# Kernel tuning notes

Measured on AMD Instinct MI355X. Metric: run time of the kernel, lower is better.

The kernel has to match this reference:

```python
import jax, jax.numpy as jnp
import numpy as np

EPS = 1e-6
CHI2_THRESH = 9.0
DIST_SCALE = 3.0


def _normalize(x, axis=1, eps=EPS):
    n = jnp.linalg.norm(x, axis=axis, keepdims=True)
    return x / jnp.maximum(n, eps)


def _skew(k):
    # k: (B,3) -> (B,3,3)
    kx, ky, kz = k[:, 0], k[:, 1], k[:, 2]
    O = jnp.zeros_like(kx)
    row0 = jnp.stack([O, -kz, ky], axis=1)
    row1 = jnp.stack([kz, O, -kx], axis=1)
    row2 = jnp.stack([-ky, kx, O], axis=1)
    return jnp.stack([row0, row1, row2], axis=1)


def gravity_align(g_src, g_tgt, eps=EPS):
    # Rodrigues rotation aligning g_src to g_tgt, batch-safe.
    u = _normalize(g_src, eps=eps)
    v = _normalize(g_tgt, eps=eps)
    axis = jnp.cross(u, v)
    axis_norm = jnp.linalg.norm(axis, axis=1, keepdims=True)
    dot = jnp.clip(jnp.sum(u * v, axis=1, keepdims=True), -1.0, 1.0)
    parallel = axis_norm < 1e-6
    k = axis / (axis_norm + eps)
    theta = jnp.arccos(dot)
    sin_t, cos_t = jnp.sin(theta), jnp.cos(theta)
    K = _skew(k)
    I = jnp.eye(3, dtype=g_src.dtype)[None]
    R = I + sin_t[:, :, None] * K + (1.0 - cos_t)[:, :, None] * (K @ K)
    # anti-parallel branch (computed unconditionally, selected via where)
    ex = jnp.array([1.0, 0.0, 0.0], dtype=u.dtype)[None]
    ey = jnp.array([0.0, 1.0, 0.0], dtype=u.dtype)[None]
    use_ex = jnp.abs(u[:, 0:1]) < 0.9
    basis = jnp.where(use_ex, ex, ey)
    axis2 = _normalize(jnp.cross(u, basis), eps=eps)
    K2 = _skew(axis2)
    R_anti = I + 2.0 * (K2 @ K2)
    antipar = parallel & (dot < 0.0)
    R = jnp.where(antipar[:, :, None], R_anti, R)
    R = jnp.where((parallel & (dot > 0.0))[:, :, None], I, R)
    return R


def _lower_median(x, axis):
    # torch.median(dim): lower median for even length
    n = x.shape[axis]
    return jnp.sort(x, axis=axis).take(indices=(n - 1) // 2, axis=axis)


def setup_inputs() -> dict:
    key = jax.random.key(0)
    ks = jax.random.split(key, 8)
    B, N = 4, 4096
    src = jax.random.normal(ks[0], (B, 3, N), jnp.float32)
    tgt = jax.random.normal(ks[1], (B, 3, N), jnp.float32)
    src_n = _normalize(jax.random.normal(ks[2], (B, 3, N), jnp.float32))
    tgt_n = _normalize(jax.random.normal(ks[3], (B, 3, N), jnp.float32))
    g_p = jax.random.normal(ks[4], (B, 3), jnp.float32)
    g_q = jax.random.normal(ks[5], (B, 3), jnp.float32)
    k_p = jax.random.uniform(ks[6], (B, 1), jnp.float32) + 0.1
    k_q = jax.random.uniform(ks[7], (B, 1), jnp.float32) + 0.1
    return {"src": src, "tgt": tgt, "src_n": src_n, "tgt_n": tgt_n,
            "g_p": g_p, "k_p": k_p, "g_q": g_q, "k_q": k_q}


def reference(src, tgt, src_n, tgt_n, g_p, k_p, g_q, k_q):
    B, _, N = src.shape
    R_g = gravity_align(g_p, g_q)  # (B,3,3)
    src_rot = jnp.einsum('bij,bjn->bin', R_g, src)
    src_n_rot = jnp.einsum('bij,bjn->bin', R_g, src_n)
    t_center = tgt.mean(axis=2, keepdims=True) - src_rot.mean(axis=2, keepdims=True)
    src_init = src_rot + t_center  # (B,3,N)

    # squared pairwise distances: (B,N,N)
    inner = -2.0 * jnp.einsum('bcn,bcm->bnm', src_init, tgt)
    xx = jnp.sum(src_init ** 2, axis=1)[:, :, None]
    yy = jnp.sum(tgt ** 2, axis=1)[:, None, :]
    dist_pq = xx + inner + yy

    min_pq = jnp.min(dist_pq, axis=2)
    corr_p2q = jnp.argmin(dist_pq, axis=2)
    min_qp = jnp.min(dist_pq, axis=1)
    corr_q2p = jnp.argmin(dist_pq, axis=1)

    nn_d_p = jnp.sqrt(jnp.maximum(min_pq, 0.0) + EPS)
    nn_d_q = jnp.sqrt(jnp.maximum(min_qp, 0.0) + EPS)
    tau_p = DIST_SCALE * _lower_median(nn_d_p, axis=1)[:, None]
    tau_q = DIST_SCALE * _lower_median(nn_d_q, axis=1)[:, None]
    geom_p = (nn_d_p <= tau_p).astype(src.dtype)
    geom_q = (nn_d_q <= tau_q).astype(src.dtype)

    tgt_n_matched_for_p = jnp.take_along_axis(tgt_n, corr_p2q[:, None, :], axis=2)
    src_n_matched_for_q = jnp.take_along_axis(src_n_rot, corr_q2p[:, None, :], axis=2)

    gq = g_q[:, :, None]
    inc_p = jnp.sum(src_n_rot * gq, axis=1)
    inc_p_ref = jnp.sum(tgt_n_matched_for_p * gq, axis=1)
    inc_q = jnp.sum(tgt_n * gq, axis=1)
    inc_q_ref = jnp.sum(src_n_matched_for_q * gq, axis=1)

    k_eff = k_p * k_q / (k_p + k_q + EPS)  # (B,1), broadcasts over N
    w_p = jax.nn.sigmoid(CHI2_THRESH - k_eff * (inc_p - inc_p_ref) ** 2) * geom_p
    w_q = jax.nn.sigmoid(CHI2_THRESH - k_eff * (inc_q - inc_q_ref) ** 2) * geom_q
    return w_p[:, None, :], w_q[:, None, :]
```

## Files before the change

kernel.cpp:

```cpp
#include <hip/hip_runtime.h>
#include <math.h>

#define NPTS 4096
#define NB 4
#define EPSF 1e-6f

__device__ __forceinline__ void gravity_align_rt(
    const float* __restrict__ g_p, const float* __restrict__ g_q,
    const float* sums, int b, float* R_out, float* t_out) {
    float gpx = g_p[3 * b + 0], gpy = g_p[3 * b + 1], gpz = g_p[3 * b + 2];
    float gqx = g_q[3 * b + 0], gqy = g_q[3 * b + 1], gqz = g_q[3 * b + 2];
    float nu = sqrtf(gpx * gpx + gpy * gpy + gpz * gpz);
    float du = fmaxf(nu, EPSF);
    float ux = gpx / du, uy = gpy / du, uz = gpz / du;
    float nv = sqrtf(gqx * gqx + gqy * gqy + gqz * gqz);
    float dv = fmaxf(nv, EPSF);
    float vx = gqx / dv, vy = gqy / dv, vz = gqz / dv;

    float ax = uy * vz - uz * vy;
    float ay = uz * vx - ux * vz;
    float az = ux * vy - uy * vx;
    float an = sqrtf(ax * ax + ay * ay + az * az);
    float dot = ux * vx + uy * vy + uz * vz;
    dot = fminf(1.0f, fmaxf(-1.0f, dot));
    bool parallel = (an < 1e-6f);

    float kx = ax / (an + EPSF), ky = ay / (an + EPSF), kz = az / (an + EPSF);
    float theta = acosf(dot);
    float st = sinf(theta), ct = cosf(theta);

    float K[9] = {0.f, -kz, ky,  kz, 0.f, -kx,  -ky, kx, 0.f};
    float KK[9];
    for (int i = 0; i < 3; ++i)
        for (int j = 0; j < 3; ++j) {
            float s2 = 0.f;
            for (int l = 0; l < 3; ++l) s2 += K[i * 3 + l] * K[l * 3 + j];
            KK[i * 3 + j] = s2;
        }
    float R[9];
    for (int i = 0; i < 9; ++i) {
        float I = (i == 0 || i == 4 || i == 8) ? 1.f : 0.f;
        R[i] = I + st * K[i] + (1.f - ct) * KK[i];
    }
    if (parallel) {
        if (dot < 0.f) {
            float bx, by, bz;
            if (fabsf(ux) < 0.9f) { bx = 1.f; by = 0.f; bz = 0.f; }
            else                  { bx = 0.f; by = 1.f; bz = 0.f; }
            float cx = uy * bz - uz * by;
            float cy = uz * bx - ux * bz;
            float cz = ux * by - uy * bx;
            float cn = sqrtf(cx * cx + cy * cy + cz * cz);
            float cd = fmaxf(cn, EPSF);
            cx /= cd; cy /= cd; cz /= cd;
            float K2[9] = {0.f, -cz, cy,  cz, 0.f, -cx,  -cy, cx, 0.f};
            float K2K2[9];
            for (int i = 0; i < 3; ++i)
                for (int j = 0; j < 3; ++j) {
                    float s2 = 0.f;
                    for (int l = 0; l < 3; ++l) s2 += K2[i * 3 + l] * K2[l * 3 + j];
                    K2K2[i * 3 + j] = s2;
                }
            for (int i = 0; i < 9; ++i) {
                float I = (i == 0 || i == 4 || i == 8) ? 1.f : 0.f;
                R[i] = I + 2.f * K2K2[i];
            }
        } else if (dot > 0.f) {
            for (int i = 0; i < 9; ++i) R[i] = (i == 0 || i == 4 || i == 8) ? 1.f : 0.f;
        }
    }
    float ms0 = sums[0] / (float)NPTS, ms1 = sums[1] / (float)NPTS, ms2 = sums[2] / (float)NPTS;
    float mt0 = sums[3] / (float)NPTS, mt1 = sums[4] / (float)NPTS, mt2 = sums[5] / (float)NPTS;
    for (int i = 0; i < 9; ++i) R_out[i] = R[i];
    t_out[0] = mt0 - (R[0] * ms0 + R[1] * ms1 + R[2] * ms2);
    t_out[1] = mt1 - (R[3] * ms0 + R[4] * ms1 + R[5] * ms2);
    t_out[2] = mt2 - (R[6] * ms0 + R[7] * ms1 + R[8] * ms2);
}

__device__ __forceinline__ void block_means_rt(
    const float* __restrict__ S, const float* __restrict__ T,
    const float* __restrict__ g_p, const float* __restrict__ g_q,
    int b, int tid, float* sf) {
    float acc[6] = {0.f, 0.f, 0.f, 0.f, 0.f, 0.f};
    if (tid < 256) {
        for (int n = tid; n < NPTS; n += 256) {
            acc[0] += S[n]; acc[1] += S[NPTS + n]; acc[2] += S[2 * NPTS + n];
            acc[3] += T[n]; acc[4] += T[NPTS + n]; acc[5] += T[2 * NPTS + n];
        }
    }
    if (tid < 256) {
        #pragma unroll
        for (int c = 0; c < 6; ++c) sf[c * 256 + tid] = acc[c];
    }
    __syncthreads();
    for (int s = 128; s > 0; s >>= 1) {
        if (tid < s) {
            #pragma unroll
            for (int c = 0; c < 6; ++c) sf[c * 256 + tid] += sf[c * 256 + tid + s];
        }
        __syncthreads();
    }
    if (tid == 0) {
        float sums[6];
        #pragma unroll
        for (int c = 0; c < 6; ++c) sums[c] = sf[c * 256];
        gravity_align_rt(g_p, g_q, sums, b, sf + 1536, sf + 1545);
    }
    __syncthreads();
}

__global__ __launch_bounds__(1024, 8) void kA(
    const float* __restrict__ src, const float* __restrict__ tgt,
    const float* __restrict__ g_p, const float* __restrict__ g_q,
    float* __restrict__ nnp, int* __restrict__ idxp,
    float* __restrict__ nnq, int* __restrict__ idxq) {
    const int b = blockIdx.y;
    const int z = blockIdx.z;
    const int tid = threadIdx.x;
    const float* S = src + (size_t)b * 3 * NPTS;
    const float* T = tgt + (size_t)b * 3 * NPTS;

    __shared__ float4 stage4[NPTS];
    float* sf = (float*)stage4;

    block_means_rt(S, T, g_p, g_q, b, tid, sf);
    const float R0 = sf[1536], R1 = sf[1537], R2 = sf[1538];
    const float R3 = sf[1539], R4 = sf[1540], R5 = sf[1541];
    const float R6 = sf[1542], R7 = sf[1543], R8 = sf[1544];
    const float t0 = sf[1545], t1 = sf[1546], t2 = sf[1547];
    __syncthreads();

    const int nl = tid & 63;
    const int stripe = tid >> 6;
    const int n = blockIdx.x * 64 + nl;
    float4 p;

    if (z == 0) {
        for (int i = tid; i < NPTS; i += 1024) {
            float q0 = T[i], q1 = T[NPTS + i], q2 = T[2 * NPTS + i];
            float w = (q0 * q0 + q1 * q1 + q2 * q2) * -0.5f;
            stage4[i] = make_float4(q0, q1, q2, w);
        }
        float s0 = S[n], s1 = S[NPTS + n], s2 = S[2 * NPTS + n];
        float p0 = R0 * s0 + R1 * s1 + R2 * s2 + t0;
        float p1 = R3 * s0 + R4 * s1 + R5 * s2 + t1;
        float p2 = R6 * s0 + R7 * s1 + R8 * s2 + t2;
        p = make_float4(p0, p1, p2, p0 * p0 + p1 * p1 + p2 * p2);
    } else {
        for (int i = tid; i < NPTS; i += 1024) {
            float s0 = S[i], s1 = S[NPTS + i], s2 = S[2 * NPTS + i];
            float p0 = R0 * s0 + R1 * s1 + R2 * s2 + t0;
            float p1 = R3 * s0 + R4 * s1 + R5 * s2 + t1;
            float p2 = R6 * s0 + R7 * s1 + R8 * s2 + t2;
            float w = (p0 * p0 + p1 * p1 + p2 * p2) * -0.5f;
            stage4[i] = make_float4(p0, p1, p2, w);
        }
        float q0 = T[n], q1 = T[NPTS + n], q2 = T[2 * NPTS + n];
        p = make_float4(q0, q1, q2, q0 * q0 + q1 * q1 + q2 * q2);
    }
    __syncthreads();

    const int m0 = stripe << 8;
    float best = -3.4e38f;
    int bi = m0;
    #pragma unroll 8
    for (int m = m0; m < m0 + 256; ++m) {
        float4 q = stage4[m];
        float s = fmaf(p.x, q.x, fmaf(p.y, q.y, fmaf(p.z, q.z, q.w)));
        if (s > best) { best = s; bi = m; }
    }
    __syncthreads();

    float* combd = sf;
    int* combi = (int*)(combd + 1024);
    combd[tid] = best;
    combi[tid] = bi;
    __syncthreads();
    if (stripe == 0) {
        for (int s2 = 1; s2 < 16; ++s2) {
            float d2 = combd[s2 * 64 + nl];
            int i2 = combi[s2 * 64 + nl];
            if (d2 > best) { best = d2; bi = i2; }
        }
        float d = fmaf(-2.0f, best, p.w);
        float* nn = z ? nnq : nnp;
        int* idx = z ? idxq : idxp;
        nn[b * NPTS + n] = sqrtf(fmaxf(d, 0.f) + EPSF);
        idx[b * NPTS + n] = bi;
    }
}

__global__ __launch_bounds__(1024, 8) void kB(
    const float* __restrict__ src, const float* __restrict__ tgt,
    const float* __restrict__ nnp, const float* __restrict__ nnq,
    const int* __restrict__ idxp, const int* __restrict__ idxq,
    const float* __restrict__ src_n, const float* __restrict__ tgt_n,
    const float* __restrict__ g_p, const float* __restrict__ g_q,
    const float* __restrict__ k_p, const float* __restrict__ k_q,
    float* __restrict__ out) {
    const int x = blockIdx.x;
    const int b = blockIdx.y;
    const int z = blockIdx.z;
    const int tid = threadIdx.x;
    const int wid = tid >> 6;
    const int lane = tid & 63;
    const float* S = src + (size_t)b * 3 * NPTS;
    const float* T = tgt + (size_t)b * 3 * NPTS;
    const float* a = (z ? nnq : nnp) + b * NPTS;

    __shared__ float msc[1548];
    __shared__ int hist[16][256];
    __shared__ int tot[256];
    __shared__ int digit_s, base_s;

    block_means_rt(S, T, g_p, g_q, b, tid, msc);
    const float R0 = msc[1536], R1 = msc[1537], R2 = msc[1538];
    const float R3 = msc[1539], R4 = msc[1540], R5 = msc[1541];
    const float R6 = msc[1542], R7 = msc[1543], R8 = msc[1544];

    unsigned int v[4];
    #pragma unroll
    for (int j = 0; j < 4; ++j)
        v[j] = __float_as_uint(a[tid + j * 1024]);

    const int shifts[4]   = {23, 15, 7, 0};
    const unsigned him[4] = {0x00000000u, 0x7F800000u, 0x7FFF8000u, 0x7FFFFF80u};
    const unsigned dm[4]  = {0xFFu, 0xFFu, 0xFFu, 0x7Fu};

    unsigned int prefix = 0u;
    int rank = 2047;

    for (int p = 0; p < 4; ++p) {
        const int sh = shifts[p];
        const unsigned himask = him[p];
        const unsigned dmask = dm[p];

        for (int k2 = lane; k2 < 256; k2 += 64) hist[wid][k2] = 0;
        __syncthreads();

        #pragma unroll
        for (int j = 0; j < 4; ++j) {
            if ((v[j] & himask) == prefix)
                atomicAdd(&hist[wid][(v[j] >> sh) & dmask], 1);
        }
        __syncthreads();

        if (tid < 256) {
            int t = 0;
            #pragma unroll
            for (int w = 0; w < 16; ++w) t += hist[w][tid];
            tot[tid] = t;
        }
        __syncthreads();

        if (wid == 0) {
            int c0 = tot[4 * lane + 0], c1 = tot[4 * lane + 1];
            int c2 = tot[4 * lane + 2], c3 = tot[4 * lane + 3];
            int s = c0 + c1 + c2 + c3;
            int incl = s;
            #pragma unroll
            for (int o = 1; o < 64; o <<= 1) {
                int t = __shfl_up(incl, o, 64);
                if (lane >= o) incl += t;
            }
            int base = incl - s;
            int cs[4] = {c0, c1, c2, c3};
            #pragma unroll
            for (int k2 = 0; k2 < 4; ++k2) {
                if (cs[k2] > 0 && rank >= base && rank < base + cs[k2]) {
                    digit_s = 4 * lane + k2;
                    base_s = base;
                }
                base += cs[k2];
            }
        }
        __syncthreads();
        prefix |= ((unsigned)digit_s) << sh;
        rank -= base_s;
        __syncthreads();
    }
    const float tauv = 3.0f * __uint_as_float(prefix);

    if (tid < 64) {
        const int n = x * 64 + tid;
        const float* SN = src_n + (size_t)b * 3 * NPTS;
        const float* TN = tgt_n + (size_t)b * 3 * NPTS;
        const float gx = g_q[3 * b + 0], gy = g_q[3 * b + 1], gz = g_q[3 * b + 2];
        const float kp = k_p[b], kq = k_q[b];
        const float keff = kp * kq / (kp + kq + EPSF);

        float w;
        if (z == 0) {
            float a0 = SN[n], a1 = SN[NPTS + n], a2 = SN[2 * NPTS + n];
            float snx = R0 * a0 + R1 * a1 + R2 * a2;
            float sny = R3 * a0 + R4 * a1 + R5 * a2;
            float snz = R6 * a0 + R7 * a1 + R8 * a2;
            float inc = snx * gx + sny * gy + snz * gz;
            int jj = idxp[b * NPTS + n];
            float tnx = TN[jj], tny = TN[NPTS + jj], tnz = TN[2 * NPTS + jj];
            float incr = tnx * gx + tny * gy + tnz * gz;
            float diff = inc - incr;
            float arg = 9.0f - keff * diff * diff;
            float sig = 1.f / (1.f + expf(-arg));
            float geom = (a[n] <= tauv) ? 1.f : 0.f;
            w = sig * geom;
        } else {
            float tnx = TN[n], tny = TN[NPTS + n], tnz = TN[2 * NPTS + n];
            float inc = tnx * gx + tny * gy + tnz * gz;
            int jj = idxq[b * NPTS + n];
            float a0 = SN[jj], a1 = SN[NPTS + jj], a2 = SN[2 * NPTS + jj];
            float snx = R0 * a0 + R1 * a1 + R2 * a2;
            float sny = R3 * a0 + R4 * a1 + R5 * a2;
            float snz = R6 * a0 + R7 * a1 + R8 * a2;
            float incr = snx * gx + sny * gy + snz * gz;
            float diff = inc - incr;
            float arg = 9.0f - keff * diff * diff;
            float sig = 1.f / (1.f + expf(-arg));
            float geom = (a[n] <= tauv) ? 1.f : 0.f;
            w = sig * geom;
        }
        out[z * (NB * NPTS) + b * NPTS + n] = w;
    }
}

extern "C" void kernel_launch(void* const* d_in, const int* in_sizes, int n_in,
                              void* d_out, int out_size, void* d_ws, size_t ws_size,
                              hipStream_t stream) {
    const float* src   = (const float*)d_in[0];
    const float* tgt   = (const float*)d_in[1];
    const float* src_n = (const float*)d_in[2];
    const float* tgt_n = (const float*)d_in[3];
    const float* g_p   = (const float*)d_in[4];
    const float* k_p   = (const float*)d_in[5];
    const float* g_q   = (const float*)d_in[6];
    const float* k_q   = (const float*)d_in[7];
    float* out = (float*)d_out;

    const int BN = NB * NPTS;
    float* nnp = (float*)d_ws;
    float* nnq = nnp + BN;
    int* idxp = (int*)(nnq + BN);
    int* idxq = idxp + BN;

    kA<<<dim3(NPTS / 64, NB, 2), dim3(1024), 0, stream>>>(src, tgt, g_p, g_q,
                                                          nnp, idxp, nnq, idxq);
    kB<<<dim3(NPTS / 64, NB, 2), dim3(1024), 0, stream>>>(src, tgt, nnp, nnq,
                                                          idxp, idxq, src_n, tgt_n,
                                                          g_p, g_q, k_p, k_q, out);
}
```

Measured before the change: 47.88 us.

## Split NN search over candidate halves and process two queries per thread

The nearest-neighbour kernel now splits the candidate set into two halves across grid z. Each thread scores two query points against each staged candidate, which halves the LDS footprint and reuses every shared-memory load twice. Partial best values and indices for each half, plus query norms, are written to workspace. The second kernel merges the halves and computes the distances. This aims to cut LDS reads per FMA and per-block shared memory, at the cost of extra global traffic and recomputing the merge in kB.

Result: no change. 48.48 us (+1.3%).

```diff
diff --git a/kernel.cpp b/kernel.cpp
--- a/kernel.cpp
+++ b/kernel.cpp
@@ -112,15 +112,19 @@
 __global__ __launch_bounds__(1024, 8) void kA(
     const float* __restrict__ src, const float* __restrict__ tgt,
     const float* __restrict__ g_p, const float* __restrict__ g_q,
-    float* __restrict__ nnp, int* __restrict__ idxp,
-    float* __restrict__ nnq, int* __restrict__ idxq) {
+    float* __restrict__ bestv0, float* __restrict__ bestv1,
+    int* __restrict__ bidx0, int* __restrict__ bidx1,
+    float* __restrict__ pw) {
+    const int x = blockIdx.x;
     const int b = blockIdx.y;
-    const int z = blockIdx.z;
+    const int zz = blockIdx.z;
+    const int z = zz >> 1;
+    const int half = zz & 1;
     const int tid = threadIdx.x;
     const float* S = src + (size_t)b * 3 * NPTS;
     const float* T = tgt + (size_t)b * 3 * NPTS;
 
-    __shared__ float4 stage4[NPTS];
+    __shared__ float4 stage4[2048];
     float* sf = (float*)stage4;
 
     block_means_rt(S, T, g_p, g_q, b, tid, sf);
@@ -132,68 +136,102 @@
 
     const int nl = tid & 63;
     const int stripe = tid >> 6;
-    const int n = blockIdx.x * 64 + nl;
-    float4 p;
+    const int n = x * 128 + nl;
+    const int mbase = half * 2048;
+    float4 pA, pB;
 
     if (z == 0) {
-        for (int i = tid; i < NPTS; i += 1024) {
-            float q0 = T[i], q1 = T[NPTS + i], q2 = T[2 * NPTS + i];
+        for (int i = tid; i < 2048; i += 1024) {
+            const int gi = mbase + i;
+            float q0 = T[gi], q1 = T[NPTS + gi], q2 = T[2 * NPTS + gi];
             float w = (q0 * q0 + q1 * q1 + q2 * q2) * -0.5f;
             stage4[i] = make_float4(q0, q1, q2, w);
         }
-        float s0 = S[n], s1 = S[NPTS + n], s2 = S[2 * NPTS + n];
-        float p0 = R0 * s0 + R1 * s1 + R2 * s2 + t0;
-        float p1 = R3 * s0 + R4 * s1 + R5 * s2 + t1;
-        float p2 = R6 * s0 + R7 * s1 + R8 * s2 + t2;
-        p = make_float4(p0, p1, p2, p0 * p0 + p1 * p1 + p2 * p2);
+        {
+            float s0 = S[n], s1 = S[NPTS + n], s2 = S[2 * NPTS + n];
+            float p0 = R0 * s0 + R1 * s1 + R2 * s2 + t0;
+            float p1 = R3 * s0 + R4 * s1 + R5 * s2 + t1;
+            float p2 = R6 * s0 + R7 * s1 + R8 * s2 + t2;
+            pA = make_float4(p0, p1, p2, p0 * p0 + p1 * p1 + p2 * p2);
+        }
+        {
+            const int n2 = n + 64;
+            float s0 = S[n2], s1 = S[NPTS + n2], s2 = S[2 * NPTS + n2];
+            float p0 = R0 * s0 + R1 * s1 + R2 * s2 + t0;
+            float p1 = R3 * s0 + R4 * s1 + R5 * s2 + t1;
+            float p2 = R6 * s0 + R7 * s1 + R8 * s2 + t2;
+            pB = make_float4(p0, p1, p2, p0 * p0 + p1 * p1 + p2 * p2);
+        }
     } else {
-        for (int i = tid; i < NPTS; i += 1024) {
-            float s0 = S[i], s1 = S[NPTS + i], s2 = S[2 * NPTS + i];
+        for (int i = tid; i < 2048; i += 1024) {
+            const int gi = mbase + i;
+            float s0 = S[gi], s1 = S[NPTS + gi], s2 = S[2 * NPTS + gi];
             float p0 = R0 * s0 + R1 * s1 + R2 * s2 + t0;
             float p1 = R3 * s0 + R4 * s1 + R5 * s2 + t1;
             float p2 = R6 * s0 + R7 * s1 + R8 * s2 + t2;
             float w = (p0 * p0 + p1 * p1 + p2 * p2) * -0.5f;
             stage4[i] = make_float4(p0, p1, p2, w);
         }
-        float q0 = T[n], q1 = T[NPTS + n], q2 = T[2 * NPTS + n];
-        p = make_float4(q0, q1, q2, q0 * q0 + q1 * q1 + q2 * q2);
-    }
-    __syncthreads();
-
-    const int m0 = stripe << 8;
-    float best = -3.4e38f;
-    int bi = m0;
+        {
+            float q0 = T[n], q1 = T[NPTS + n], q2 = T[2 * NPTS + n];
+            pA = make_float4(q0, q1, q2, q0 * q0 + q1 * q1 + q2 * q2);
+        }
+        {
+            const int n2 = n + 64;
+            float q0 = T[n2], q1 = T[NPTS + n2], q2 = T[2 * NPTS + n2];
+            pB = make_float4(q0, q1, q2, q0 * q0 + q1 * q1 + q2 * q2);
+        }
+    }
+    __syncthreads();
+
+    const int m0 = stripe << 7;
+    float bestA = -3.4e38f, bestB = -3.4e38f;
+    int biA = m0, biB = m0;
     #pragma unroll 8
-    for (int m = m0; m < m0 + 256; ++m) {
+    for (int m = m0; m < m0 + 128; ++m) {
         float4 q = stage4[m];
-        float s = fmaf(p.x, q.x, fmaf(p.y, q.y, fmaf(p.z, q.z, q.w)));
-        if (s > best) { best = s; bi = m; }
+        float sA = fmaf(pA.x, q.x, fmaf(pA.y, q.y, fmaf(pA.z, q.z, q.w)));
+        float sB = fmaf(pB.x, q.x, fmaf(pB.y, q.y, fmaf(pB.z, q.z, q.w)));
+        if (sA > bestA) { bestA = sA; biA = m; }
+        if (sB > bestB) { bestB = sB; biB = m; }
     }
     __syncthreads();
 
     float* combd = sf;
-    int* combi = (int*)(combd + 1024);
-    combd[tid] = best;
-    combi[tid] = bi;
+    int* combi = (int*)(sf + 2048);
+    combd[tid] = bestA;
+    combd[1024 + tid] = bestB;
+    combi[tid] = biA;
+    combi[1024 + tid] = biB;
     __syncthreads();
     if (stripe == 0) {
         for (int s2 = 1; s2 < 16; ++s2) {
-            float d2 = combd[s2 * 64 + nl];
-            int i2 = combi[s2 * 64 + nl];
-            if (d2 > best) { best = d2; bi = i2; }
-        }
-        float d = fmaf(-2.0f, best, p.w);
-        float* nn = z ? nnq : nnp;
-        int* idx = z ? idxq : idxp;
-        nn[b * NPTS + n] = sqrtf(fmaxf(d, 0.f) + EPSF);
-        idx[b * NPTS + n] = bi;
+            float dA = combd[s2 * 64 + nl];
+            int iA = combi[s2 * 64 + nl];
+            if (dA > bestA) { bestA = dA; biA = iA; }
+            float dB = combd[1024 + s2 * 64 + nl];
+            int iB = combi[1024 + s2 * 64 + nl];
+            if (dB > bestB) { bestB = dB; biB = iB; }
+        }
+        const size_t off = (size_t)(z * NB + b) * NPTS;
+        float* bv = half ? bestv1 : bestv0;
+        int* bx = half ? bidx1 : bidx0;
+        bv[off + n] = bestA;
+        bv[off + n + 64] = bestB;
+        bx[off + n] = mbase + biA;
+        bx[off + n + 64] = mbase + biB;
+        if (half == 0) {
+            pw[off + n] = pA.w;
+            pw[off + n + 64] = pB.w;
+        }
     }
 }
 
 __global__ __launch_bounds__(1024, 8) void kB(
     const float* __restrict__ src, const float* __restrict__ tgt,
-    const float* __restrict__ nnp, const float* __restrict__ nnq,
-    const int* __restrict__ idxp, const int* __restrict__ idxq,
+    const float* __restrict__ bestv0, const float* __restrict__ bestv1,
+    const int* __restrict__ bidx0, const int* __restrict__ bidx1,
+    const float* __restrict__ pw,
     const float* __restrict__ src_n, const float* __restrict__ tgt_n,
     const float* __restrict__ g_p, const float* __restrict__ g_q,
     const float* __restrict__ k_p, const float* __restrict__ k_q,
@@ -206,7 +244,7 @@
     const int lane = tid & 63;
     const float* S = src + (size_t)b * 3 * NPTS;
     const float* T = tgt + (size_t)b * 3 * NPTS;
-    const float* a = (z ? nnq : nnp) + b * NPTS;
+    const size_t off = (size_t)(z * NB + b) * NPTS;
 
     __shared__ float msc[1548];
     __shared__ int hist[16][256];
@@ -220,8 +258,14 @@
 
     unsigned int v[4];
     #pragma unroll
-    for (int j = 0; j < 4; ++j)
-        v[j] = __float_as_uint(a[tid + j * 1024]);
+    for (int j = 0; j < 4; ++j) {
+        const int n = tid + j * 1024;
+        float s0 = bestv0[off + n], s1 = bestv1[off + n];
+        float sb = (s1 > s0) ? s1 : s0;
+        float d = fmaf(-2.0f, sb, pw[off + n]);
+        float nv = sqrtf(fmaxf(d, 0.f) + EPSF);
+        v[j] = __float_as_uint(nv);
+    }
 
     const int shifts[4]   = {23, 15, 7, 0};
     const unsigned him[4] = {0x00000000u, 0x7F800000u, 0x7FFF8000u, 0x7FFFFF80u};
@@ -283,6 +327,13 @@
 
     if (tid < 64) {
         const int n = x * 64 + tid;
+        float s0 = bestv0[off + n], s1 = bestv1[off + n];
+        bool takeB = (s1 > s0);
+        float sb = takeB ? s1 : s0;
+        int jj = takeB ? bidx1[off + n] : bidx0[off + n];
+        float d = fmaf(-2.0f, sb, pw[off + n]);
+        float nv = sqrtf(fmaxf(d, 0.f) + EPSF);
+
         const float* SN = src_n + (size_t)b * 3 * NPTS;
         const float* TN = tgt_n + (size_t)b * 3 * NPTS;
         const float gx = g_q[3 * b + 0], gy = g_q[3 * b + 1], gz = g_q[3 * b + 2];
@@ -296,18 +347,16 @@
             float sny = R3 * a0 + R4 * a1 + R5 * a2;
             float snz = R6 * a0 + R7 * a1 + R8 * a2;
             float inc = snx * gx + sny * gy + snz * gz;
-            int jj = idxp[b * NPTS + n];
             float tnx = TN[jj], tny = TN[NPTS + jj], tnz = TN[2 * NPTS + jj];
             float incr = tnx * gx + tny * gy + tnz * gz;
             float diff = inc - incr;
             float arg = 9.0f - keff * diff * diff;
             float sig = 1.f / (1.f + expf(-arg));
-            float geom = (a[n] <= tauv) ? 1.f : 0.f;
+            float geom = (nv <= tauv) ? 1.f : 0.f;
             w = sig * geom;
         } else {
             float tnx = TN[n], tny = TN[NPTS + n], tnz = TN[2 * NPTS + n];
             float inc = tnx * gx + tny * gy + tnz * gz;
-            int jj = idxq[b * NPTS + n];
             float a0 = SN[jj], a1 = SN[NPTS + jj], a2 = SN[2 * NPTS + jj];
             float snx = R0 * a0 + R1 * a1 + R2 * a2;
             float sny = R3 * a0 + R4 * a1 + R5 * a2;
@@ -316,7 +365,7 @@
             float diff = inc - incr;
             float arg = 9.0f - keff * diff * diff;
             float sig = 1.f / (1.f + expf(-arg));
-            float geom = (a[n] <= tauv) ? 1.f : 0.f;
+            float geom = (nv <= tauv) ? 1.f : 0.f;
             w = sig * geom;
         }
         out[z * (NB * NPTS) + b * NPTS + n] = w;
@@ -336,15 +385,17 @@
     const float* k_q   = (const float*)d_in[7];
     float* out = (float*)d_out;
 
-    const int BN = NB * NPTS;
-    float* nnp = (float*)d_ws;
-    float* nnq = nnp + BN;
-    int* idxp = (int*)(nnq + BN);
-    int* idxq = idxp + BN;
-
-    kA<<<dim3(NPTS / 64, NB, 2), dim3(1024), 0, stream>>>(src, tgt, g_p, g_q,
-                                                          nnp, idxp, nnq, idxq);
-    kB<<<dim3(NPTS / 64, NB, 2), dim3(1024), 0, stream>>>(src, tgt, nnp, nnq,
-                                                          idxp, idxq, src_n, tgt_n,
-                                                          g_p, g_q, k_p, k_q, out);
+    const int BN = 2 * NB * NPTS;
+    float* bestv0 = (float*)d_ws;
+    float* bestv1 = bestv0 + BN;
+    int* bidx0 = (int*)(bestv1 + BN);
+    int* bidx1 = bidx0 + BN;
+    float* pw = (float*)(bidx1 + BN);
+
+    kA<<<dim3(32, NB, 4), dim3(1024), 0, stream>>>(src, tgt, g_p, g_q,
+                                                   bestv0, bestv1, bidx0, bidx1, pw);
+    kB<<<dim3(NPTS / 64, NB, 2), dim3(1024), 0, stream>>>(src, tgt,
+                                                          bestv0, bestv1, bidx0, bidx1, pw,
+                                                          src_n, tgt_n, g_p, g_q,
+                                                          k_p, k_q, out);
 }
```

## Precompute transformed packed point arrays in a separate kernel, stream them from global memory

Applied to the files above, without the earlier changes.

Adds a pack kernel that computes the per-batch centroid alignment transform once and writes packed float4 arrays (coordinates plus squared norm) for both clouds to workspace. The nearest-neighbour kernel then drops its redundant per-block mean reduction and LDS staging, and reads candidates directly from global memory through a wave-uniform (readfirstlane) pointer so the loads can go through the scalar or cached path. This removes the repeated reduction across all 512 blocks and the shared-memory fill, at the cost of an extra kernel launch and a pack kernel that only runs 4 blocks.

Result: slower. 66.37 us (+38.6%).

```diff
diff --git a/kernel.cpp b/kernel.cpp
--- a/kernel.cpp
+++ b/kernel.cpp
@@ -109,70 +109,69 @@
     __syncthreads();
 }
 
-__global__ __launch_bounds__(1024, 8) void kA(
+__global__ __launch_bounds__(1024, 8) void kPack(
     const float* __restrict__ src, const float* __restrict__ tgt,
     const float* __restrict__ g_p, const float* __restrict__ g_q,
+    float4* __restrict__ Pown, float4* __restrict__ Pstage,
+    float4* __restrict__ Qown, float4* __restrict__ Qstage) {
+    const int b = blockIdx.x;
+    const int tid = threadIdx.x;
+    const float* S = src + (size_t)b * 3 * NPTS;
+    const float* T = tgt + (size_t)b * 3 * NPTS;
+
+    __shared__ float sf[1548];
+    block_means_rt(S, T, g_p, g_q, b, tid, sf);
+    const float R0 = sf[1536], R1 = sf[1537], R2 = sf[1538];
+    const float R3 = sf[1539], R4 = sf[1540], R5 = sf[1541];
+    const float R6 = sf[1542], R7 = sf[1543], R8 = sf[1544];
+    const float t0 = sf[1545], t1 = sf[1546], t2 = sf[1547];
+
+    for (int n = tid; n < NPTS; n += 1024) {
+        float s0 = S[n], s1 = S[NPTS + n], s2 = S[2 * NPTS + n];
+        float p0 = R0 * s0 + R1 * s1 + R2 * s2 + t0;
+        float p1 = R3 * s0 + R4 * s1 + R5 * s2 + t1;
+        float p2 = R6 * s0 + R7 * s1 + R8 * s2 + t2;
+        float pp = p0 * p0 + p1 * p1 + p2 * p2;
+        Pown[b * NPTS + n] = make_float4(p0, p1, p2, pp);
+        Pstage[b * NPTS + n] = make_float4(p0, p1, p2, (p0 * p0 + p1 * p1 + p2 * p2) * -0.5f);
+
+        float q0 = T[n], q1 = T[NPTS + n], q2 = T[2 * NPTS + n];
+        float qq = q0 * q0 + q1 * q1 + q2 * q2;
+        Qown[b * NPTS + n] = make_float4(q0, q1, q2, qq);
+        Qstage[b * NPTS + n] = make_float4(q0, q1, q2, (q0 * q0 + q1 * q1 + q2 * q2) * -0.5f);
+    }
+}
+
+__global__ __launch_bounds__(1024, 8) void kA(
+    const float4* __restrict__ Pown, const float4* __restrict__ Pstage,
+    const float4* __restrict__ Qown, const float4* __restrict__ Qstage,
     float* __restrict__ nnp, int* __restrict__ idxp,
     float* __restrict__ nnq, int* __restrict__ idxq) {
     const int b = blockIdx.y;
     const int z = blockIdx.z;
     const int tid = threadIdx.x;
-    const float* S = src + (size_t)b * 3 * NPTS;
-    const float* T = tgt + (size_t)b * 3 * NPTS;
-
-    __shared__ float4 stage4[NPTS];
-    float* sf = (float*)stage4;
-
-    block_means_rt(S, T, g_p, g_q, b, tid, sf);
-    const float R0 = sf[1536], R1 = sf[1537], R2 = sf[1538];
-    const float R3 = sf[1539], R4 = sf[1540], R5 = sf[1541];
-    const float R6 = sf[1542], R7 = sf[1543], R8 = sf[1544];
-    const float t0 = sf[1545], t1 = sf[1546], t2 = sf[1547];
-    __syncthreads();
+    const float4* own = z ? Qown : Pown;
+    const float4* stg = z ? Pstage : Qstage;
 
     const int nl = tid & 63;
     const int stripe = tid >> 6;
     const int n = blockIdx.x * 64 + nl;
-    float4 p;
-
-    if (z == 0) {
-        for (int i = tid; i < NPTS; i += 1024) {
-            float q0 = T[i], q1 = T[NPTS + i], q2 = T[2 * NPTS + i];
-            float w = (q0 * q0 + q1 * q1 + q2 * q2) * -0.5f;
-            stage4[i] = make_float4(q0, q1, q2, w);
-        }
-        float s0 = S[n], s1 = S[NPTS + n], s2 = S[2 * NPTS + n];
-        float p0 = R0 * s0 + R1 * s1 + R2 * s2 + t0;
-        float p1 = R3 * s0 + R4 * s1 + R5 * s2 + t1;
-        float p2 = R6 * s0 + R7 * s1 + R8 * s2 + t2;
-        p = make_float4(p0, p1, p2, p0 * p0 + p1 * p1 + p2 * p2);
-    } else {
-        for (int i = tid; i < NPTS; i += 1024) {
-            float s0 = S[i], s1 = S[NPTS + i], s2 = S[2 * NPTS + i];
-            float p0 = R0 * s0 + R1 * s1 + R2 * s2 + t0;
-            float p1 = R3 * s0 + R4 * s1 + R5 * s2 + t1;
-            float p2 = R6 * s0 + R7 * s1 + R8 * s2 + t2;
-            float w = (p0 * p0 + p1 * p1 + p2 * p2) * -0.5f;
-            stage4[i] = make_float4(p0, p1, p2, w);
-        }
-        float q0 = T[n], q1 = T[NPTS + n], q2 = T[2 * NPTS + n];
-        p = make_float4(q0, q1, q2, q0 * q0 + q1 * q1 + q2 * q2);
-    }
-    __syncthreads();
-
-    const int m0 = stripe << 8;
+    const float4 p = own[b * NPTS + n];
+
+    const int m0u = __builtin_amdgcn_readfirstlane(stripe << 8);
+    const float4* sb = stg + b * NPTS + m0u;
+
     float best = -3.4e38f;
-    int bi = m0;
-    #pragma unroll 8
-    for (int m = m0; m < m0 + 256; ++m) {
-        float4 q = stage4[m];
+    int bi = m0u;
+    #pragma unroll 4
+    for (int m = 0; m < 256; ++m) {
+        float4 q = sb[m];
         float s = fmaf(p.x, q.x, fmaf(p.y, q.y, fmaf(p.z, q.z, q.w)));
-        if (s > best) { best = s; bi = m; }
-    }
-    __syncthreads();
-
-    float* combd = sf;
-    int* combi = (int*)(combd + 1024);
+        if (s > best) { best = s; bi = m0u + m; }
+    }
+
+    __shared__ float combd[1024];
+    __shared__ int combi[1024];
     combd[tid] = best;
     combi[tid] = bi;
     __syncthreads();
@@ -337,12 +336,18 @@
     float* out = (float*)d_out;
 
     const int BN = NB * NPTS;
-    float* nnp = (float*)d_ws;
+    float4* Pown   = (float4*)d_ws;
+    float4* Pstage = Pown + BN;
+    float4* Qown   = Pstage + BN;
+    float4* Qstage = Qown + BN;
+    float* nnp = (float*)(Qstage + BN);
     float* nnq = nnp + BN;
     int* idxp = (int*)(nnq + BN);
     int* idxq = idxp + BN;
 
-    kA<<<dim3(NPTS / 64, NB, 2), dim3(1024), 0, stream>>>(src, tgt, g_p, g_q,
+    kPack<<<dim3(NB), dim3(1024), 0, stream>>>(src, tgt, g_p, g_q,
+                                               Pown, Pstage, Qown, Qstage);
+    kA<<<dim3(NPTS / 64, NB, 2), dim3(1024), 0, stream>>>(Pown, Pstage, Qown, Qstage,
                                                           nnp, idxp, nnq, idxq);
     kB<<<dim3(NPTS / 64, NB, 2), dim3(1024), 0, stream>>>(src, tgt, nnp, nnq,
                                                           idxp, idxq, src_n, tgt_n,
```
